# Optimization experiments

Hardware: AMD Instinct MI355X
Metric: run time of the kernel (lower is better)

The kernel has to match this reference:

```python
import jax, jax.numpy as jnp
import numpy as np

NUM_LAYERS = 4


def setup_inputs() -> dict:
    key = jax.random.key(0)
    k1, k2, k3, k4 = jax.random.split(key, 4)
    num_users, num_items, D, E = 100000, 50000, 64, 2000000
    N = num_users + num_items
    emb_users = jax.random.normal(k1, (num_users, D), dtype=jnp.float32)
    emb_items = jax.random.normal(k2, (num_items, D), dtype=jnp.float32)
    src = jax.random.randint(k3, (E,), 0, N, dtype=jnp.int64)
    dst = jax.random.randint(k4, (E,), 0, N, dtype=jnp.int64)
    edge_index = jnp.stack([src, dst], axis=0)
    return {"emb_users": emb_users, "emb_items": emb_items, "edge_index": edge_index}


def _lightgcn(emb_users, emb_items, edge_index):
    num_users = emb_users.shape[0]
    num_items = emb_items.shape[0]
    N = num_users + num_items
    src, dst = edge_index[0], edge_index[1]

    # gcn_norm without self-loops (PyG LGConv default): deg over destination nodes
    ones = jnp.ones(src.shape[0], dtype=emb_users.dtype)
    deg = jax.ops.segment_sum(ones, dst, num_segments=N)
    deg_inv_sqrt = jnp.where(deg > 0, jax.lax.rsqrt(jnp.maximum(deg, 1.0)), 0.0)
    norm = deg_inv_sqrt[src] * deg_inv_sqrt[dst]  # [E]

    emb = jnp.concatenate([emb_users, emb_items], axis=0)  # [N, D]
    acc = emb
    for _ in range(NUM_LAYERS):
        msg = norm[:, None] * emb[src]  # [E, D]
        emb = jax.ops.segment_sum(msg, dst, num_segments=N)
        acc = acc + emb

    # original: 1/(L+1) * mean(stack, dim=1) == sum / (L+1)^2
    emb_final = acc / float((NUM_LAYERS + 1) ** 2)
    return emb_final[:num_users], emb_final[num_users:]


def reference(emb_users, emb_items, edge_index):
    return _lightgcn(emb_users, emb_items, edge_index)
```

## Files before the change

### kernel.cpp

```cpp
#include <hip/hip_runtime.h>
#include <hip/hip_bf16.h>

#define D 64
#define NUM_LAYERS 4
#define TILE 4096
#define EPT 16
#define BKMAX 320


__global__ void bhist_kernel(const int* __restrict__ dst, int* __restrict__ bcnt, int E, int nbk) {
    __shared__ int h[BKMAX];
    for (int i = threadIdx.x; i < nbk; i += blockDim.x) h[i] = 0;
    __syncthreads();
    int stride = gridDim.x * blockDim.x;
    for (int e = blockIdx.x * blockDim.x + threadIdx.x; e < E; e += stride)
        atomicAdd(&h[dst[e] >> 9], 1);
    __syncthreads();
    for (int i = threadIdx.x; i < nbk; i += blockDim.x)
        if (h[i] > 0) atomicAdd(&bcnt[i], h[i]);
}

__global__ __launch_bounds__(512) void bscan_kernel(const int* __restrict__ bcnt,
                                                    int* __restrict__ bstart,
                                                    int* __restrict__ gcur, int nbk, int E) {
    __shared__ int sm[512];
    int t = threadIdx.x;
    int v = (t < nbk) ? bcnt[t] : 0;
    sm[t] = v;
    __syncthreads();
    for (int ofs = 1; ofs < 512; ofs <<= 1) {
        int x = (t >= ofs) ? sm[t - ofs] : 0;
        __syncthreads();
        sm[t] += x;
        __syncthreads();
    }
    int excl = sm[t] - v;
    if (t < nbk) { bstart[t] = excl; gcur[t] = excl; }
    if (t == 0) bstart[nbk] = E;
}


__global__ __launch_bounds__(256) void placeA_kernel(const int* __restrict__ src,
                                                     const int* __restrict__ dst,
                                                     int* __restrict__ gcur,
                                                     int* __restrict__ mid,
                                                     int E, int nbk) {
    __shared__ int hist[BKMAX];
    __shared__ int gbase[BKMAX];
    int t = threadIdx.x;
    int tile0 = blockIdx.x * TILE;
    for (int i = t; i < nbk; i += 256) hist[i] = 0;
    __syncthreads();

    int p_[EPT];
    int b_[EPT];
    int r_[EPT];
#pragma unroll
    for (int i = 0; i < EPT; ++i) {
        int e = tile0 + i * 256 + t;
        b_[i] = -1;
        if (e < E) {
            int s = src[e], d = dst[e];
            p_[i] = s | ((d & 511) << 18);
            b_[i] = d >> 9;
            r_[i] = atomicAdd(&hist[b_[i]], 1);
        }
    }
    __syncthreads();
    for (int b = t; b < nbk; b += 256) {
        int h = hist[b];
        gbase[b] = (h > 0) ? atomicAdd(&gcur[b], h) : 0;
    }
    __syncthreads();
#pragma unroll
    for (int i = 0; i < EPT; ++i) {
        if (b_[i] >= 0) mid[gbase[b_[i]] + r_[i]] = p_[i];
    }
}

__global__ __launch_bounds__(512) void placeB1_kernel(const int* __restrict__ bstart,
                                                      const int* __restrict__ mid,
                                                      int* __restrict__ row_start,
                                                      float* __restrict__ dis,
                                                      int N, int nbk, int E) {
    __shared__ int degsm[512];
    __shared__ int sc[512];
    int b = blockIdx.x;
    int t = threadIdx.x;
    int node0 = b << 9;
    int lo = bstart[b], hi = bstart[b + 1];
    degsm[t] = 0;
    __syncthreads();
    for (int e = lo + t; e < hi; e += 512)
        atomicAdd(&degsm[(mid[e] >> 18) & 511], 1);
    __syncthreads();
    int d = degsm[t];
    sc[t] = d;
    __syncthreads();
    for (int ofs = 1; ofs < 512; ofs <<= 1) {
        int x = (t >= ofs) ? sc[t - ofs] : 0;
        __syncthreads();
        sc[t] += x;
        __syncthreads();
    }
    int excl = sc[t] - d;
    int node = node0 + t;
    if (node < N) {
        row_start[node] = lo + excl;
        dis[node] = (d > 0) ? rsqrtf((float)d) : 0.0f;
    }
    if (b == nbk - 1 && t == 0) row_start[N] = E;
}

__global__ __launch_bounds__(512) void placeB2_kernel(const int* __restrict__ bstart,
                                                      const int* __restrict__ mid,
                                                      const int* __restrict__ row_start,
                                                      const float* __restrict__ dis,
                                                      int2* __restrict__ csr, int N) {
    __shared__ int cur[512];
    __shared__ float dloc[512];
    int b = blockIdx.x;
    int t = threadIdx.x;
    int node0 = b << 9;
    int node = node0 + t;
    if (node < N) { cur[t] = row_start[node]; dloc[t] = dis[node]; }
    else          { cur[t] = 0; dloc[t] = 0.0f; }
    __syncthreads();
    int lo = bstart[b], hi = bstart[b + 1];
    for (int e = lo + t; e < hi; e += 512) {
        int m = mid[e];
        int l = (m >> 18) & 511;
        int s = m & 0x3FFFF;
        float w = dis[s] * dloc[l];
        int slot = atomicAdd(&cur[l], 1);
        csr[slot] = make_int2(s, __float_as_int(w));
    }
}


__global__ void init_kernel(const float* __restrict__ users, const float* __restrict__ items,
                            unsigned* __restrict__ A, int nu_elems, int total2) {
    int i = blockIdx.x * blockDim.x + threadIdx.x;
    if (i >= total2) return;
    int base = i * 2;
    float2 v;
    if (base < nu_elems) v = ((const float2*)users)[i];
    else                 v = ((const float2*)items)[(base - nu_elems) >> 1];
    __hip_bfloat16 bx = __float2bfloat16(v.x);
    __hip_bfloat16 by = __float2bfloat16(v.y);
    unsigned p = (unsigned)(*reinterpret_cast<unsigned short*>(&bx))
               | ((unsigned)(*reinterpret_cast<unsigned short*>(&by)) << 16);
    A[i] = p;
}

__device__ __forceinline__ float bf_lo(unsigned u) { return __uint_as_float(u << 16); }
__device__ __forceinline__ float bf_hi(unsigned u) { return __uint_as_float(u & 0xffff0000u); }
__device__ __forceinline__ unsigned bf_pack(float x, float y) {
    __hip_bfloat16 bx = __float2bfloat16(x);
    __hip_bfloat16 by = __float2bfloat16(y);
    return (unsigned)(*reinterpret_cast<unsigned short*>(&bx))
         | ((unsigned)(*reinterpret_cast<unsigned short*>(&by)) << 16);
}

template <int FINAL>
__global__ void gather_kernel(const int* __restrict__ row_start,
                              const int2* __restrict__ csr,
                              const uint2* __restrict__ Au,
                              uint2* __restrict__ Bu,
                              const float* __restrict__ users, const float* __restrict__ items,
                              const uint2* __restrict__ L1u, const uint2* __restrict__ L2u,
                              float* __restrict__ out,
                              int N, int nu) {
    int node = (blockIdx.x * blockDim.x + threadIdx.x) >> 6;
    if (node >= N) return;
    int lane = threadIdx.x & 63;
    int q = lane >> 4;
    int c = lane & 15;
    int beg = row_start[node];
    int end = row_start[node + 1];
    int deg = end - beg;
    float ax = 0.0f, ay = 0.0f, az = 0.0f, aw = 0.0f;

    for (int base = 0; base < deg; base += 64) {
        int chunk = min(64, deg - base);
        int   sl = 0;
        float wl = 0.0f;
        if (lane < chunk) {
            int2 e = csr[beg + base + lane];
            sl = e.x;
            wl = __int_as_float(e.y);
        }
        int k = 0;
        for (; k + 8 <= chunk; k += 8) {
            int i0 = k + q, i1 = k + 4 + q;
            int   s0 = __shfl(sl, i0), s1 = __shfl(sl, i1);
            float w0 = __shfl(wl, i0), w1 = __shfl(wl, i1);
            uint2 u0 = Au[(size_t)s0 * 16 + c];
            uint2 u1 = Au[(size_t)s1 * 16 + c];
            ax += w0 * bf_lo(u0.x); ay += w0 * bf_hi(u0.x);
            az += w0 * bf_lo(u0.y); aw += w0 * bf_hi(u0.y);
            ax += w1 * bf_lo(u1.x); ay += w1 * bf_hi(u1.x);
            az += w1 * bf_lo(u1.y); aw += w1 * bf_hi(u1.y);
        }
        for (; k < chunk; k += 4) {
            int i0 = k + q;
            int   s = __shfl(sl, i0);
            float w = __shfl(wl, i0);
            uint2 u = Au[(size_t)s * 16 + c];
            ax += w * bf_lo(u.x); ay += w * bf_hi(u.x);
            az += w * bf_lo(u.y); aw += w * bf_hi(u.y);
        }
    }

    ax += __shfl_xor(ax, 16); ay += __shfl_xor(ay, 16);
    az += __shfl_xor(az, 16); aw += __shfl_xor(aw, 16);
    ax += __shfl_xor(ax, 32); ay += __shfl_xor(ay, 32);
    az += __shfl_xor(az, 32); aw += __shfl_xor(aw, 32);

    if (q == 0) {
        size_t ro = (size_t)node * 16 + c;
        if (FINAL) {
            uint2 l1 = L1u[ro], l2 = L2u[ro], l3 = Au[ro];
            float4 e0;
            if (node < nu) e0 = ((const float4*)users)[ro];
            else           e0 = ((const float4*)items)[(size_t)(node - nu) * 16 + c];
            float rx = (e0.x + bf_lo(l1.x) + bf_lo(l2.x) + bf_lo(l3.x) + ax) * 0.04f;
            float ry = (e0.y + bf_hi(l1.x) + bf_hi(l2.x) + bf_hi(l3.x) + ay) * 0.04f;
            float rz = (e0.z + bf_lo(l1.y) + bf_lo(l2.y) + bf_lo(l3.y) + az) * 0.04f;
            float rw = (e0.w + bf_hi(l1.y) + bf_hi(l2.y) + bf_hi(l3.y) + aw) * 0.04f;
            ((float4*)out)[ro] = make_float4(rx, ry, rz, rw);
        } else {
            uint2 p;
            p.x = bf_pack(ax, ay);
            p.y = bf_pack(az, aw);
            Bu[ro] = p;
        }
    }
}


extern "C" void kernel_launch(void* const* d_in, const int* in_sizes, int n_in,
                              void* d_out, int out_size, void* d_ws, size_t ws_size,
                              hipStream_t stream) {
    const float* users = (const float*)d_in[0];
    const float* items = (const float*)d_in[1];
    const int*   eidx  = (const int*)d_in[2];

    const int nu = in_sizes[0] / D;
    const int ni = in_sizes[1] / D;
    const int N  = nu + ni;
    const int E  = in_sizes[2] / 2;
    const int Nf = N * D;
    const int nbk = (N + 511) >> 9;

    const int* src = eidx;
    const int* dst = eidx + E;

    char* ws = (char*)d_ws;
    size_t off = 0;
    auto alloc = [&](size_t bytes) {
        char* p = ws + off;
        off += (bytes + 255) & ~(size_t)255;
        return p;
    };
    float* dis       = (float*)alloc((size_t)N * 4);
    int*   row_start = (int*)alloc((size_t)(N + 1) * 4);
    int*   bcnt      = (int*)alloc(BKMAX * 4);
    int*   bstart    = (int*)alloc((BKMAX + 1) * 4);
    int*   gcur      = (int*)alloc(BKMAX * 4);
    int2*  csr       = (int2*)alloc((size_t)E * 8);
    unsigned* A0 = (unsigned*)alloc((size_t)Nf * 2);
    unsigned* L1 = (unsigned*)alloc((size_t)Nf * 2);
    unsigned* L2 = (unsigned*)alloc((size_t)Nf * 2);
    unsigned* L3 = (unsigned*)alloc((size_t)Nf * 2);
    int* mid = (int*)L3;

    const int B256 = 256;
    auto blocks = [](long long n, int b) { return (int)((n + b - 1) / b); };

    hipMemsetAsync(bcnt, 0, BKMAX * 4, stream);
    bhist_kernel<<<1024, B256, 0, stream>>>(dst, bcnt, E, nbk);
    bscan_kernel<<<1, 512, 0, stream>>>(bcnt, bstart, gcur, nbk, E);

    placeA_kernel<<<blocks(E, TILE), B256, 0, stream>>>(src, dst, gcur, mid, E, nbk);
    placeB1_kernel<<<nbk, 512, 0, stream>>>(bstart, mid, row_start, dis, N, nbk, E);
    placeB2_kernel<<<nbk, 512, 0, stream>>>(bstart, mid, row_start, dis, csr, N);

    init_kernel<<<blocks(Nf / 2, B256), B256, 0, stream>>>(users, items, A0, nu * D, Nf / 2);

    const int ggrid = blocks(N, B256 / 64);
    gather_kernel<0><<<ggrid, B256, 0, stream>>>(row_start, csr, (const uint2*)A0, (uint2*)L1,
                                                 nullptr, nullptr, nullptr, nullptr, nullptr, N, nu);
    gather_kernel<0><<<ggrid, B256, 0, stream>>>(row_start, csr, (const uint2*)L1, (uint2*)L2,
                                                 nullptr, nullptr, nullptr, nullptr, nullptr, N, nu);
    gather_kernel<0><<<ggrid, B256, 0, stream>>>(row_start, csr, (const uint2*)L2, (uint2*)L3,
                                                 nullptr, nullptr, nullptr, nullptr, nullptr, N, nu);
    gather_kernel<1><<<ggrid, B256, 0, stream>>>(row_start, csr, (const uint2*)L3, nullptr,
                                                 users, items, (const uint2*)L1, (const uint2*)L2,
                                                 (float*)d_out, N, nu);
}
```

Measured before the change: 403.4 us.

## Map one node per 16 lanes in gather with 4-way unrolled edge loop

The gather kernel now assigns 16 lanes per destination node instead of a full 64-lane wavefront, so each wave processes four nodes. Each group walks its edge list directly with a 4-way unroll and independent accumulators, replacing the shuffle-based broadcast and the cross-quarter reduction. CSR entries and the L1/L2 reads in the final layer use nontemporal loads. This cuts idle lanes on low-degree nodes (average degree is about 13) and removes shuffle overhead, at the cost of divergence when nodes in the same wave have different degrees.

Result: slower. 427.4 us (+5.9%).

```diff
diff --git a/kernel.cpp b/kernel.cpp
--- a/kernel.cpp
+++ b/kernel.cpp
@@ -163,7 +163,7 @@
 }
 
 template <int FINAL>
-__global__ void gather_kernel(const int* __restrict__ row_start,
+__global__ __launch_bounds__(256) void gather_kernel(const int* __restrict__ row_start,
                               const int2* __restrict__ csr,
                               const uint2* __restrict__ Au,
                               uint2* __restrict__ Bu,
@@ -171,70 +171,77 @@
                               const uint2* __restrict__ L1u, const uint2* __restrict__ L2u,
                               float* __restrict__ out,
                               int N, int nu) {
-    int node = (blockIdx.x * blockDim.x + threadIdx.x) >> 6;
+    int node = (blockIdx.x * blockDim.x + threadIdx.x) >> 4;
     if (node >= N) return;
-    int lane = threadIdx.x & 63;
-    int q = lane >> 4;
-    int c = lane & 15;
+    int c = threadIdx.x & 15;
     int beg = row_start[node];
     int end = row_start[node + 1];
-    int deg = end - beg;
-    float ax = 0.0f, ay = 0.0f, az = 0.0f, aw = 0.0f;
-
-    for (int base = 0; base < deg; base += 64) {
-        int chunk = min(64, deg - base);
-        int   sl = 0;
-        float wl = 0.0f;
-        if (lane < chunk) {
-            int2 e = csr[beg + base + lane];
-            sl = e.x;
-            wl = __int_as_float(e.y);
-        }
-        int k = 0;
-        for (; k + 8 <= chunk; k += 8) {
-            int i0 = k + q, i1 = k + 4 + q;
-            int   s0 = __shfl(sl, i0), s1 = __shfl(sl, i1);
-            float w0 = __shfl(wl, i0), w1 = __shfl(wl, i1);
-            uint2 u0 = Au[(size_t)s0 * 16 + c];
-            uint2 u1 = Au[(size_t)s1 * 16 + c];
-            ax += w0 * bf_lo(u0.x); ay += w0 * bf_hi(u0.x);
-            az += w0 * bf_lo(u0.y); aw += w0 * bf_hi(u0.y);
-            ax += w1 * bf_lo(u1.x); ay += w1 * bf_hi(u1.x);
-            az += w1 * bf_lo(u1.y); aw += w1 * bf_hi(u1.y);
-        }
-        for (; k < chunk; k += 4) {
-            int i0 = k + q;
-            int   s = __shfl(sl, i0);
-            float w = __shfl(wl, i0);
-            uint2 u = Au[(size_t)s * 16 + c];
-            ax += w * bf_lo(u.x); ay += w * bf_hi(u.x);
-            az += w * bf_lo(u.y); aw += w * bf_hi(u.y);
-        }
-    }
-
-    ax += __shfl_xor(ax, 16); ay += __shfl_xor(ay, 16);
-    az += __shfl_xor(az, 16); aw += __shfl_xor(aw, 16);
-    ax += __shfl_xor(ax, 32); ay += __shfl_xor(ay, 32);
-    az += __shfl_xor(az, 32); aw += __shfl_xor(aw, 32);
-
-    if (q == 0) {
-        size_t ro = (size_t)node * 16 + c;
-        if (FINAL) {
-            uint2 l1 = L1u[ro], l2 = L2u[ro], l3 = Au[ro];
-            float4 e0;
-            if (node < nu) e0 = ((const float4*)users)[ro];
-            else           e0 = ((const float4*)items)[(size_t)(node - nu) * 16 + c];
-            float rx = (e0.x + bf_lo(l1.x) + bf_lo(l2.x) + bf_lo(l3.x) + ax) * 0.04f;
-            float ry = (e0.y + bf_hi(l1.x) + bf_hi(l2.x) + bf_hi(l3.x) + ay) * 0.04f;
-            float rz = (e0.z + bf_lo(l1.y) + bf_lo(l2.y) + bf_lo(l3.y) + az) * 0.04f;
-            float rw = (e0.w + bf_hi(l1.y) + bf_hi(l2.y) + bf_hi(l3.y) + aw) * 0.04f;
-            ((float4*)out)[ro] = make_float4(rx, ry, rz, rw);
-        } else {
-            uint2 p;
-            p.x = bf_pack(ax, ay);
-            p.y = bf_pack(az, aw);
-            Bu[ro] = p;
-        }
+
+    const long long* csr64 = (const long long*)csr;
+
+    float ax0 = 0.f, ay0 = 0.f, az0 = 0.f, aw0 = 0.f;
+    float ax1 = 0.f, ay1 = 0.f, az1 = 0.f, aw1 = 0.f;
+    float ax2 = 0.f, ay2 = 0.f, az2 = 0.f, aw2 = 0.f;
+    float ax3 = 0.f, ay3 = 0.f, az3 = 0.f, aw3 = 0.f;
+
+    for (int j = beg; j < end; j += 4) {
+        int last = end - 1;
+        int j1 = min(j + 1, last);
+        int j2 = min(j + 2, last);
+        int j3 = min(j + 3, last);
+        long long p0 = __builtin_nontemporal_load(csr64 + j);
+        long long p1 = __builtin_nontemporal_load(csr64 + j1);
+        long long p2 = __builtin_nontemporal_load(csr64 + j2);
+        long long p3 = __builtin_nontemporal_load(csr64 + j3);
+        int s0 = (int)(p0 & 0xFFFFFFFFLL);
+        int s1 = (int)(p1 & 0xFFFFFFFFLL);
+        int s2 = (int)(p2 & 0xFFFFFFFFLL);
+        int s3 = (int)(p3 & 0xFFFFFFFFLL);
+        uint2 u0 = Au[(size_t)s0 * 16 + c];
+        uint2 u1 = Au[(size_t)s1 * 16 + c];
+        uint2 u2 = Au[(size_t)s2 * 16 + c];
+        uint2 u3 = Au[(size_t)s3 * 16 + c];
+        float w0 = __int_as_float((int)(p0 >> 32));
+        float w1 = (j + 1 < end) ? __int_as_float((int)(p1 >> 32)) : 0.0f;
+        float w2 = (j + 2 < end) ? __int_as_float((int)(p2 >> 32)) : 0.0f;
+        float w3 = (j + 3 < end) ? __int_as_float((int)(p3 >> 32)) : 0.0f;
+        ax0 += w0 * bf_lo(u0.x); ay0 += w0 * bf_hi(u0.x);
+        az0 += w0 * bf_lo(u0.y); aw0 += w0 * bf_hi(u0.y);
+        ax1 += w1 * bf_lo(u1.x); ay1 += w1 * bf_hi(u1.x);
+        az1 += w1 * bf_lo(u1.y); aw1 += w1 * bf_hi(u1.y);
+        ax2 += w2 * bf_lo(u2.x); ay2 += w2 * bf_hi(u2.x);
+        az2 += w2 * bf_lo(u2.y); aw2 += w2 * bf_hi(u2.y);
+        ax3 += w3 * bf_lo(u3.x); ay3 += w3 * bf_hi(u3.x);
+        az3 += w3 * bf_lo(u3.y); aw3 += w3 * bf_hi(u3.y);
+    }
+
+    float ax = (ax0 + ax1) + (ax2 + ax3);
+    float ay = (ay0 + ay1) + (ay2 + ay3);
+    float az = (az0 + az1) + (az2 + az3);
+    float aw = (aw0 + aw1) + (aw2 + aw3);
+
+    size_t ro = (size_t)node * 16 + c;
+    if (FINAL) {
+        uint2 l1;
+        l1.x = __builtin_nontemporal_load(&L1u[ro].x);
+        l1.y = __builtin_nontemporal_load(&L1u[ro].y);
+        uint2 l2;
+        l2.x = __builtin_nontemporal_load(&L2u[ro].x);
+        l2.y = __builtin_nontemporal_load(&L2u[ro].y);
+        uint2 l3 = Au[ro];
+        float4 e0;
+        if (node < nu) e0 = ((const float4*)users)[ro];
+        else           e0 = ((const float4*)items)[(size_t)(node - nu) * 16 + c];
+        float rx = (e0.x + bf_lo(l1.x) + bf_lo(l2.x) + bf_lo(l3.x) + ax) * 0.04f;
+        float ry = (e0.y + bf_hi(l1.x) + bf_hi(l2.x) + bf_hi(l3.x) + ay) * 0.04f;
+        float rz = (e0.z + bf_lo(l1.y) + bf_lo(l2.y) + bf_lo(l3.y) + az) * 0.04f;
+        float rw = (e0.w + bf_hi(l1.y) + bf_hi(l2.y) + bf_hi(l3.y) + aw) * 0.04f;
+        ((float4*)out)[ro] = make_float4(rx, ry, rz, rw);
+    } else {
+        uint2 p;
+        p.x = bf_pack(ax, ay);
+        p.y = bf_pack(az, aw);
+        Bu[ro] = p;
     }
 }
 
@@ -288,7 +295,7 @@
 
     init_kernel<<<blocks(Nf / 2, B256), B256, 0, stream>>>(users, items, A0, nu * D, Nf / 2);
 
-    const int ggrid = blocks(N, B256 / 64);
+    const int ggrid = blocks((long long)N * 16, B256);
     gather_kernel<0><<<ggrid, B256, 0, stream>>>(row_start, csr, (const uint2*)A0, (uint2*)L1,
                                                  nullptr, nullptr, nullptr, nullptr, nullptr, N, nu);
     gather_kernel<0><<<ggrid, B256, 0, stream>>>(row_start, csr, (const uint2*)L1, (uint2*)L2,
```

## Compute per-node degrees in histogram pass and merge CSR placement kernels

Applied to the files above, without the earlier changes.

Per-node degree counting moves into the bucket-histogram kernel through global atomics, which lets the two placeB kernels merge into one that scans degrees and computes normalization inline. Edge loads in the histogram and placement kernels are vectorized to int4, and the bf16 init kernel now handles 8 floats per thread. The aim is to remove a kernel launch plus one pass over the mid buffer and the dis array. In exchange it adds 2M global atomics on deg and a random deg[s] read per edge with an rsqrt recomputed for every edge.

Measured after the change: 462.2 us. 14.6% more time.

```diff
diff --git a/kernel.cpp b/kernel.cpp
--- a/kernel.cpp
+++ b/kernel.cpp
@@ -8,13 +8,36 @@
 #define BKMAX 320
 
 
-__global__ void bhist_kernel(const int* __restrict__ dst, int* __restrict__ bcnt, int E, int nbk) {
+__device__ __forceinline__ float bf_lo(unsigned u) { return __uint_as_float(u << 16); }
+__device__ __forceinline__ float bf_hi(unsigned u) { return __uint_as_float(u & 0xffff0000u); }
+__device__ __forceinline__ unsigned bf_pack(float x, float y) {
+    __hip_bfloat16 bx = __float2bfloat16(x);
+    __hip_bfloat16 by = __float2bfloat16(y);
+    return (unsigned)(*reinterpret_cast<unsigned short*>(&bx))
+         | ((unsigned)(*reinterpret_cast<unsigned short*>(&by)) << 16);
+}
+
+
+__global__ void bhist_kernel(const int* __restrict__ dst, int* __restrict__ bcnt,
+                             int* __restrict__ deg, int E, int nbk) {
     __shared__ int h[BKMAX];
     for (int i = threadIdx.x; i < nbk; i += blockDim.x) h[i] = 0;
     __syncthreads();
     int stride = gridDim.x * blockDim.x;
-    for (int e = blockIdx.x * blockDim.x + threadIdx.x; e < E; e += stride)
-        atomicAdd(&h[dst[e] >> 9], 1);
+    int gid = blockIdx.x * blockDim.x + threadIdx.x;
+    int E4 = (((size_t)dst & 15) == 0) ? (E >> 2) : 0;
+    const int4* dst4 = (const int4*)dst;
+    for (int i = gid; i < E4; i += stride) {
+        int4 d = dst4[i];
+        atomicAdd(&h[d.x >> 9], 1); atomicAdd(&deg[d.x], 1);
+        atomicAdd(&h[d.y >> 9], 1); atomicAdd(&deg[d.y], 1);
+        atomicAdd(&h[d.z >> 9], 1); atomicAdd(&deg[d.z], 1);
+        atomicAdd(&h[d.w >> 9], 1); atomicAdd(&deg[d.w], 1);
+    }
+    for (int e = (E4 << 2) + gid; e < E; e += stride) {
+        int d = dst[e];
+        atomicAdd(&h[d >> 9], 1); atomicAdd(&deg[d], 1);
+    }
     __syncthreads();
     for (int i = threadIdx.x; i < nbk; i += blockDim.x)
         if (h[i] > 0) atomicAdd(&bcnt[i], h[i]);
@@ -52,18 +75,37 @@
     for (int i = t; i < nbk; i += 256) hist[i] = 0;
     __syncthreads();
 
+    bool al = (((size_t)src & 15) == 0) && (((size_t)dst & 15) == 0);
+
     int p_[EPT];
     int b_[EPT];
     int r_[EPT];
 #pragma unroll
-    for (int i = 0; i < EPT; ++i) {
-        int e = tile0 + i * 256 + t;
-        b_[i] = -1;
-        if (e < E) {
-            int s = src[e], d = dst[e];
-            p_[i] = s | ((d & 511) << 18);
-            b_[i] = d >> 9;
-            r_[i] = atomicAdd(&hist[b_[i]], 1);
+    for (int i4 = 0; i4 < 4; ++i4) {
+        int e0 = tile0 + i4 * 1024 + t * 4;
+        int4 s4, d4;
+        if (al && (e0 + 3 < E)) {
+            s4 = *(const int4*)(src + e0);
+            d4 = *(const int4*)(dst + e0);
+        } else {
+            s4 = make_int4(0, 0, 0, 0); d4 = make_int4(0, 0, 0, 0);
+            if (e0     < E) { s4.x = src[e0];     d4.x = dst[e0]; }
+            if (e0 + 1 < E) { s4.y = src[e0 + 1]; d4.y = dst[e0 + 1]; }
+            if (e0 + 2 < E) { s4.z = src[e0 + 2]; d4.z = dst[e0 + 2]; }
+            if (e0 + 3 < E) { s4.w = src[e0 + 3]; d4.w = dst[e0 + 3]; }
+        }
+        int ss[4] = { s4.x, s4.y, s4.z, s4.w };
+        int dd[4] = { d4.x, d4.y, d4.z, d4.w };
+#pragma unroll
+        for (int k = 0; k < 4; ++k) {
+            int i = i4 * 4 + k;
+            int e = e0 + k;
+            b_[i] = -1;
+            if (e < E) {
+                p_[i] = ss[k] | ((dd[k] & 511) << 18);
+                b_[i] = dd[k] >> 9;
+                r_[i] = atomicAdd(&hist[b_[i]], 1);
+            }
         }
     }
     __syncthreads();
@@ -78,60 +120,41 @@
     }
 }
 
-__global__ __launch_bounds__(512) void placeB1_kernel(const int* __restrict__ bstart,
-                                                      const int* __restrict__ mid,
-                                                      int* __restrict__ row_start,
-                                                      float* __restrict__ dis,
-                                                      int N, int nbk, int E) {
-    __shared__ int degsm[512];
+__global__ __launch_bounds__(512) void placeB_kernel(const int* __restrict__ bstart,
+                                                     const int* __restrict__ mid,
+                                                     const int* __restrict__ deg,
+                                                     int* __restrict__ row_start,
+                                                     int2* __restrict__ csr,
+                                                     int N, int nbk, int E) {
     __shared__ int sc[512];
-    int b = blockIdx.x;
-    int t = threadIdx.x;
-    int node0 = b << 9;
-    int lo = bstart[b], hi = bstart[b + 1];
-    degsm[t] = 0;
-    __syncthreads();
-    for (int e = lo + t; e < hi; e += 512)
-        atomicAdd(&degsm[(mid[e] >> 18) & 511], 1);
-    __syncthreads();
-    int d = degsm[t];
-    sc[t] = d;
-    __syncthreads();
-    for (int ofs = 1; ofs < 512; ofs <<= 1) {
-        int x = (t >= ofs) ? sc[t - ofs] : 0;
-        __syncthreads();
-        sc[t] += x;
-        __syncthreads();
-    }
-    int excl = sc[t] - d;
-    int node = node0 + t;
-    if (node < N) {
-        row_start[node] = lo + excl;
-        dis[node] = (d > 0) ? rsqrtf((float)d) : 0.0f;
-    }
-    if (b == nbk - 1 && t == 0) row_start[N] = E;
-}
-
-__global__ __launch_bounds__(512) void placeB2_kernel(const int* __restrict__ bstart,
-                                                      const int* __restrict__ mid,
-                                                      const int* __restrict__ row_start,
-                                                      const float* __restrict__ dis,
-                                                      int2* __restrict__ csr, int N) {
     __shared__ int cur[512];
     __shared__ float dloc[512];
     int b = blockIdx.x;
     int t = threadIdx.x;
     int node0 = b << 9;
     int node = node0 + t;
-    if (node < N) { cur[t] = row_start[node]; dloc[t] = dis[node]; }
-    else          { cur[t] = 0; dloc[t] = 0.0f; }
-    __syncthreads();
     int lo = bstart[b], hi = bstart[b + 1];
+    int d = (node < N) ? deg[node] : 0;
+    sc[t] = d;
+    __syncthreads();
+    for (int ofs = 1; ofs < 512; ofs <<= 1) {
+        int x = (t >= ofs) ? sc[t - ofs] : 0;
+        __syncthreads();
+        sc[t] += x;
+        __syncthreads();
+    }
+    int excl = sc[t] - d;
+    if (node < N) row_start[node] = lo + excl;
+    cur[t] = lo + excl;
+    dloc[t] = (d > 0) ? rsqrtf((float)d) : 0.0f;
+    if (b == nbk - 1 && t == 0) row_start[N] = E;
+    __syncthreads();
     for (int e = lo + t; e < hi; e += 512) {
         int m = mid[e];
         int l = (m >> 18) & 511;
         int s = m & 0x3FFFF;
-        float w = dis[s] * dloc[l];
+        int dsv = deg[s];
+        float w = ((dsv > 0) ? rsqrtf((float)dsv) : 0.0f) * dloc[l];
         int slot = atomicAdd(&cur[l], 1);
         csr[slot] = make_int2(s, __float_as_int(w));
     }
@@ -139,27 +162,21 @@
 
 
 __global__ void init_kernel(const float* __restrict__ users, const float* __restrict__ items,
-                            unsigned* __restrict__ A, int nu_elems, int total2) {
+                            unsigned* __restrict__ A, int nu_elems, int total8) {
     int i = blockIdx.x * blockDim.x + threadIdx.x;
-    if (i >= total2) return;
-    int base = i * 2;
-    float2 v;
-    if (base < nu_elems) v = ((const float2*)users)[i];
-    else                 v = ((const float2*)items)[(base - nu_elems) >> 1];
-    __hip_bfloat16 bx = __float2bfloat16(v.x);
-    __hip_bfloat16 by = __float2bfloat16(v.y);
-    unsigned p = (unsigned)(*reinterpret_cast<unsigned short*>(&bx))
-               | ((unsigned)(*reinterpret_cast<unsigned short*>(&by)) << 16);
-    A[i] = p;
-}
-
-__device__ __forceinline__ float bf_lo(unsigned u) { return __uint_as_float(u << 16); }
-__device__ __forceinline__ float bf_hi(unsigned u) { return __uint_as_float(u & 0xffff0000u); }
-__device__ __forceinline__ unsigned bf_pack(float x, float y) {
-    __hip_bfloat16 bx = __float2bfloat16(x);
-    __hip_bfloat16 by = __float2bfloat16(y);
-    return (unsigned)(*reinterpret_cast<unsigned short*>(&bx))
-         | ((unsigned)(*reinterpret_cast<unsigned short*>(&by)) << 16);
+    if (i >= total8) return;
+    long long base = (long long)i * 8;
+    const float4* p;
+    if (base < nu_elems) p = (const float4*)users + (base >> 2);
+    else                 p = (const float4*)items + ((base - nu_elems) >> 2);
+    float4 a = p[0];
+    float4 b = p[1];
+    uint4 r;
+    r.x = bf_pack(a.x, a.y);
+    r.y = bf_pack(a.z, a.w);
+    r.z = bf_pack(b.x, b.y);
+    r.w = bf_pack(b.z, b.w);
+    ((uint4*)A)[i] = r;
 }
 
 template <int FINAL>
@@ -263,9 +280,9 @@
         off += (bytes + 255) & ~(size_t)255;
         return p;
     };
-    float* dis       = (float*)alloc((size_t)N * 4);
     int*   row_start = (int*)alloc((size_t)(N + 1) * 4);
-    int*   bcnt      = (int*)alloc(BKMAX * 4);
+    int*   bcnt      = (int*)alloc(BKMAX * 4 + (size_t)N * 4);
+    int*   deg       = bcnt + BKMAX;
     int*   bstart    = (int*)alloc((BKMAX + 1) * 4);
     int*   gcur      = (int*)alloc(BKMAX * 4);
     int2*  csr       = (int2*)alloc((size_t)E * 8);
@@ -278,15 +295,14 @@
     const int B256 = 256;
     auto blocks = [](long long n, int b) { return (int)((n + b - 1) / b); };
 
-    hipMemsetAsync(bcnt, 0, BKMAX * 4, stream);
-    bhist_kernel<<<1024, B256, 0, stream>>>(dst, bcnt, E, nbk);
+    hipMemsetAsync(bcnt, 0, BKMAX * 4 + (size_t)N * 4, stream);
+    bhist_kernel<<<1024, B256, 0, stream>>>(dst, bcnt, deg, E, nbk);
     bscan_kernel<<<1, 512, 0, stream>>>(bcnt, bstart, gcur, nbk, E);
 
     placeA_kernel<<<blocks(E, TILE), B256, 0, stream>>>(src, dst, gcur, mid, E, nbk);
-    placeB1_kernel<<<nbk, 512, 0, stream>>>(bstart, mid, row_start, dis, N, nbk, E);
-    placeB2_kernel<<<nbk, 512, 0, stream>>>(bstart, mid, row_start, dis, csr, N);
-
-    init_kernel<<<blocks(Nf / 2, B256), B256, 0, stream>>>(users, items, A0, nu * D, Nf / 2);
+    placeB_kernel<<<nbk, 512, 0, stream>>>(bstart, mid, deg, row_start, csr, N, nbk, E);
+
+    init_kernel<<<blocks(Nf / 8, B256), B256, 0, stream>>>(users, items, A0, nu * D, Nf / 8);
 
     const int ggrid = blocks(N, B256 / 64);
     gather_kernel<0><<<ggrid, B256, 0, stream>>>(row_start, csr, (const uint2*)A0, (uint2*)L1,
```
